# Optimization experiments

Measured on AMD Instinct MI355X. Metric: run time of the kernel, lower is better.

## Reference

```python
import jax, jax.numpy as jnp
import numpy as np

D_MODEL = 1024
NUM_HEADS = 16
HEAD_DIM = D_MODEL // NUM_HEADS


def setup_inputs() -> dict:
    key = jax.random.key(0)
    ks = jax.random.split(key, 11)
    B, S, D = 2, 2048, D_MODEL
    s = 1.0 / np.sqrt(D)
    return {
        "query": jax.random.normal(ks[0], (B, S, D), jnp.float32),
        "key": jax.random.normal(ks[1], (B, S, D), jnp.float32),
        "value": jax.random.normal(ks[2], (B, S, D), jnp.float32),
        "W_q": jax.random.normal(ks[3], (D, D), jnp.float32) * s,
        "b_q": jnp.zeros((D,), jnp.float32),
        "W_k": jax.random.normal(ks[4], (D, D), jnp.float32) * s,
        "b_k": jnp.zeros((D,), jnp.float32),
        "W_v": jax.random.normal(ks[5], (D, D), jnp.float32) * s,
        "b_v": jnp.zeros((D,), jnp.float32),
        "W_o": jax.random.normal(ks[6], (D, D), jnp.float32) * s,
        "b_o": jnp.zeros((D,), jnp.float32),
    }


def reference(query, key, value, W_q, b_q, W_k, b_k, W_v, b_v, W_o, b_o):
    B, S, D = query.shape
    H, Dh = NUM_HEADS, HEAD_DIM
    # linear projections then split heads: [B, S, D] -> [B, H, S, Dh]
    def split_heads(x):
        return x.reshape(B, -1, H, Dh).transpose(0, 2, 1, 3)
    Q = split_heads(query @ W_q.T + b_q)
    K = split_heads(key @ W_k.T + b_k)
    V = split_heads(value @ W_v.T + b_v)
    # NOTE: original scales by d_model**-0.5, not head_dim**-0.5
    scale = jnp.asarray(D, Q.dtype) ** -0.5
    scores = jnp.einsum("bhqd,bhkd->bhqk", Q, K) * scale
    attn = jax.nn.softmax(scores, axis=-1)  # includes max-subtraction stabilization
    out = jnp.einsum("bhqk,bhkd->bhqd", attn, V)
    out = out.transpose(0, 2, 1, 3).reshape(B, -1, D)
    return out @ W_o.T + b_o
```

## Files before the change

kernel.cpp:

```cpp
#include <hip/hip_runtime.h>
#include <stdint.h>


typedef unsigned short u16;
typedef short s16x8 __attribute__((ext_vector_type(8)));
typedef short s16x4 __attribute__((ext_vector_type(4)));
typedef float f32x4 __attribute__((ext_vector_type(4)));
typedef u16 u16x4 __attribute__((ext_vector_type(4)));

#define S_LEN 2048
#define DMODEL 1024
#define LOG2E 1.44269504088896340736f

__device__ __forceinline__ u16 f2bf(float f) {
  union { float f; uint32_t u; } v; v.f = f;
  return (u16)((v.u + 0x8000u) >> 16);
}

__device__ __forceinline__ s16x8 ld8f(const float* s) {
  f32x4 a = *(const f32x4*)s;
  f32x4 b = *(const f32x4*)(s + 4);
  s16x8 r;
  r[0] = (short)f2bf(a[0]); r[1] = (short)f2bf(a[1]);
  r[2] = (short)f2bf(a[2]); r[3] = (short)f2bf(a[3]);
  r[4] = (short)f2bf(b[0]); r[5] = (short)f2bf(b[1]);
  r[6] = (short)f2bf(b[2]); r[7] = (short)f2bf(b[3]);
  return r;
}

__device__ __forceinline__ void gl2lds16(const u16* g, u16* l) {
  __builtin_amdgcn_global_load_lds(
      (const __attribute__((address_space(1))) uint32_t*)g,
      (__attribute__((address_space(3))) uint32_t*)l, 16, 0, 0);
}

struct Cvt7 { const float* s[7]; u16* d[7]; int n[7]; };

__global__ __launch_bounds__(256) void cvt7(Cvt7 p) {
  const int z = blockIdx.y;
  const int idx = blockIdx.x * 256 + threadIdx.x;
  if (idx * 8 < p.n[z])
    *(s16x8*)(p.d[z] + (size_t)idx * 8) = ld8f(p.s[z] + (size_t)idx * 8);
}

struct GemmBatch {
  const u16* A[3]; const u16* W[3]; const float* Bv[3]; void* C[3];
};

template <bool OUT_F32>
__global__ __launch_bounds__(256) void gemm_bt(GemmBatch p, int M, int N, int K) {
  __shared__ u16 As[128 * 64];
  __shared__ u16 Ws[128 * 64];
  const int z = blockIdx.z;
  const u16* __restrict__ A      = p.A[z];
  const u16* __restrict__ W      = p.W[z];
  const float* __restrict__ bias = p.Bv[z];

  const int tid = threadIdx.x;
  const int wave = tid >> 6, lane = tid & 63;
  const int quad = lane >> 4, l16 = lane & 15;
  const int bm = blockIdx.y * 128, bn = blockIdx.x * 128;
  const int wr = (wave >> 1) * 64, wc = (wave & 1) * 64;
  const int sr8 = lane >> 3;
  const int slc = (lane & 7) ^ sr8;
  const int srow = wave * 8 + sr8;

  f32x4 acc[4][4];
#pragma unroll
  for (int i = 0; i < 4; i++)
#pragma unroll
    for (int j = 0; j < 4; j++) acc[i][j] = {0.f, 0.f, 0.f, 0.f};

  const u16* Ab = A + (size_t)bm * K;
  const u16* Wb = W + (size_t)bn * K;

  for (int kt = 0; kt < K; kt += 64) {
    __syncthreads();
#pragma unroll
    for (int i = 0; i < 4; i++)
      gl2lds16(Ab + (size_t)(i * 32 + srow) * K + kt + slc * 8,
               &As[(i * 32 + wave * 8) * 64]);
#pragma unroll
    for (int i = 0; i < 4; i++)
      gl2lds16(Wb + (size_t)(i * 32 + srow) * K + kt + slc * 8,
               &Ws[(i * 32 + wave * 8) * 64]);
    __syncthreads();

#pragma unroll
    for (int ks = 0; ks < 2; ks++) {
      const int ch = ks * 4 + quad;
      s16x8 a[4], b[4];
#pragma unroll
      for (int t = 0; t < 4; t++)
        a[t] = *(const s16x8*)&As[(wr + t * 16 + l16) * 64 + ((ch ^ (l16 & 7)) << 3)];
#pragma unroll
      for (int t = 0; t < 4; t++)
        b[t] = *(const s16x8*)&Ws[(wc + t * 16 + l16) * 64 + ((ch ^ (l16 & 7)) << 3)];
#pragma unroll
      for (int i = 0; i < 4; i++)
#pragma unroll
        for (int j = 0; j < 4; j++)
          acc[i][j] = __builtin_amdgcn_mfma_f32_16x16x32_bf16(a[i], b[j], acc[i][j], 0, 0, 0);
    }
  }

#pragma unroll
  for (int j = 0; j < 4; j++) {
    const int col = bn + wc + j * 16 + l16;
    const float bv = bias[col];
#pragma unroll
    for (int i = 0; i < 4; i++) {
      const int row0 = bm + wr + i * 16 + quad * 4;
#pragma unroll
      for (int r = 0; r < 4; r++) {
        const float val = acc[i][j][r] + bv;
        if (OUT_F32)
          ((float*)p.C[z])[(size_t)(row0 + r) * N + col] = val;
        else
          ((u16*)p.C[z])[(size_t)(row0 + r) * N + col] = f2bf(val);
      }
    }
  }
}

__global__ __launch_bounds__(256) void transpose_v(const u16* __restrict__ Vp,
                                                   u16* __restrict__ Vt) {
  __shared__ u16 t[64 * 72];
  const int tid = threadIdx.x;
  const int bh = blockIdx.y, b = bh >> 4, h = bh & 15;
  const int s0 = blockIdx.x * 64;
  const int r = tid >> 4, c4 = (tid & 15) * 4;
#pragma unroll
  for (int i = 0; i < 4; i++) {
    const int s = i * 16 + r;
    u16x4 v = *(const u16x4*)&Vp[(size_t)(b * S_LEN + s0 + s) * DMODEL + h * 64 + c4];
    *(u16x4*)&t[s * 72 + c4] = v;
  }
  __syncthreads();
#pragma unroll
  for (int i = 0; i < 4; i++) {
    const int d = i * 16 + r;
    u16x4 v;
    v.x = t[(c4 + 0) * 72 + d];
    v.y = t[(c4 + 1) * 72 + d];
    v.z = t[(c4 + 2) * 72 + d];
    v.w = t[(c4 + 3) * 72 + d];
    *(u16x4*)&Vt[(size_t)(bh * 64 + d) * S_LEN + s0 + c4] = v;
  }
}

__global__ __launch_bounds__(512, 2) void attn_kernel(const u16* __restrict__ Qp,
                                                      const u16* __restrict__ Kp,
                                                      const u16* __restrict__ Vt,
                                                      u16* __restrict__ AO) {
  __shared__ u16 Qs[128 * 64];
  __shared__ u16 Ks[128 * 64];
  __shared__ u16 Vs[64 * 128];

  const int tid = threadIdx.x;
  const int wave = tid >> 6, lane = tid & 63;
  const int quad = lane >> 4, l16 = lane & 15;
  const int bh = blockIdx.y, b = bh >> 4, h = bh & 15;
  const int s0 = blockIdx.x * 128;
  const float c = 0.03125f * LOG2E;

  const int sr = tid >> 3, sc8 = tid & 7;
  const int sxor = (sc8 ^ (sr & 7)) << 3;
  const int vr = tid >> 4, vc = tid & 15;
  const int vxor = (vc ^ (vr & 15)) << 3;

#pragma unroll
  for (int i = 0; i < 2; i++) {
    const int rr = i * 64 + sr;
    s16x8 qv = *(const s16x8*)(Qp + (size_t)(b * S_LEN + s0 + rr) * DMODEL + h * 64 + sc8 * 8);
    *(s16x8*)&Qs[rr * 64 + sxor] = qv;
  }
  __syncthreads();

  s16x8 aq[2];
#pragma unroll
  for (int ks = 0; ks < 2; ks++) {
    const int ch = ks * 4 + quad;
    aq[ks] = *(const s16x8*)&Qs[(wave * 16 + l16) * 64 + ((ch ^ (l16 & 7)) << 3)];
  }

  s16x8 kv[2], vv[2];
#pragma unroll
  for (int i = 0; i < 2; i++)
    kv[i] = *(const s16x8*)(Kp + (size_t)(b * S_LEN + i * 64 + sr) * DMODEL + h * 64 + sc8 * 8);
#pragma unroll
  for (int i = 0; i < 2; i++)
    vv[i] = *(const s16x8*)(Vt + (size_t)(bh * 64 + i * 32 + vr) * S_LEN + vc * 8);

  f32x4 o[4];
  float l_r = 0.f;
#pragma unroll
  for (int dt = 0; dt < 4; dt++) o[dt] = {0.f, 0.f, 0.f, 0.f};

  const f32x4 zf = {0.f, 0.f, 0.f, 0.f};

  for (int kt = 0; kt < S_LEN; kt += 128) {
    __syncthreads();
#pragma unroll
    for (int i = 0; i < 2; i++)
      *(s16x8*)&Ks[(i * 64 + sr) * 64 + sxor] = kv[i];
#pragma unroll
    for (int i = 0; i < 2; i++)
      *(s16x8*)&Vs[(i * 32 + vr) * 128 + vxor] = vv[i];
    __syncthreads();

    if (kt + 128 < S_LEN) {
      const int k2 = kt + 128;
#pragma unroll
      for (int i = 0; i < 2; i++)
        kv[i] = *(const s16x8*)(Kp + (size_t)(b * S_LEN + k2 + i * 64 + sr) * DMODEL + h * 64 + sc8 * 8);
#pragma unroll
      for (int i = 0; i < 2; i++)
        vv[i] = *(const s16x8*)(Vt + (size_t)(bh * 64 + i * 32 + vr) * S_LEN + k2 + vc * 8);
    }

#pragma unroll
    for (int kvt = 0; kvt < 8; kvt++) {
      const int krow = kvt * 16 + l16;
      s16x8 ak0 = *(const s16x8*)&Ks[krow * 64 + (((0 + quad) ^ (l16 & 7)) << 3)];
      s16x8 ak1 = *(const s16x8*)&Ks[krow * 64 + (((4 + quad) ^ (l16 & 7)) << 3)];
      f32x4 sA;
      sA = __builtin_amdgcn_mfma_f32_16x16x32_bf16(ak0, aq[0], zf, 0, 0, 0);
      sA = __builtin_amdgcn_mfma_f32_16x16x32_bf16(ak1, aq[1], sA, 0, 0, 0);

      s16x4 pf;
      float rs = 0.f;
#pragma unroll
      for (int r = 0; r < 4; r++) {
        const float p0 = exp2f(sA[r] * c);
        rs += p0;
        pf[r] = (short)f2bf(p0);
      }
      l_r += rs;

      const int ch = kvt * 2 + (quad >> 1);
#pragma unroll
      for (int dt = 0; dt < 4; dt++) {
        const int row = dt * 16 + l16;
        s16x4 bv = *(const s16x4*)&Vs[row * 128 + ((ch ^ l16) << 3) + (quad & 1) * 4];
        o[dt] = __builtin_amdgcn_mfma_f32_16x16x16bf16_1k(pf, bv, o[dt], 0, 0, 0);
      }
    }
  }

  l_r += __shfl_xor(l_r, 16);
  l_r += __shfl_xor(l_r, 32);
#pragma unroll
  for (int r = 0; r < 4; r++) {
    const float linv = 1.f / __shfl(l_r, quad * 4 + r);
    const int row = s0 + wave * 16 + quad * 4 + r;
#pragma unroll
    for (int dt = 0; dt < 4; dt++)
      AO[(size_t)(b * S_LEN + row) * DMODEL + h * 64 + dt * 16 + l16] =
          f2bf(o[dt][r] * linv);
  }
}

extern "C" void kernel_launch(void* const* d_in, const int* in_sizes, int n_in,
                              void* d_out, int out_size, void* d_ws, size_t ws_size,
                              hipStream_t stream) {
  const float* query = (const float*)d_in[0];
  const float* key_  = (const float*)d_in[1];
  const float* value = (const float*)d_in[2];
  const float* W_q = (const float*)d_in[3];
  const float* b_q = (const float*)d_in[4];
  const float* W_k = (const float*)d_in[5];
  const float* b_k = (const float*)d_in[6];
  const float* W_v = (const float*)d_in[7];
  const float* b_v = (const float*)d_in[8];
  const float* W_o = (const float*)d_in[9];
  const float* b_o = (const float*)d_in[10];
  float* out = (float*)d_out;

  const int M = 2 * S_LEN;
  const int N = DMODEL, K = DMODEL;
  const size_t WSZ = (size_t)DMODEL * DMODEL;
  const size_t SZ  = (size_t)M * DMODEL;

  u16* Wqb = (u16*)d_ws;
  u16* Wkb = Wqb + WSZ;
  u16* Wvb = Wkb + WSZ;
  u16* Wob = Wvb + WSZ;
  u16* Qa  = Wob + WSZ;
  u16* Ka  = Qa + SZ;
  u16* Va  = Ka + SZ;
  u16* Qp  = Va + SZ;
  u16* Kp  = Qp + SZ;
  u16* Vp  = Kp + SZ;
  u16* Vt  = Qa;
  u16* AO  = Qp;

  Cvt7 cw;
  cw.s[0] = W_q;   cw.d[0] = Wqb; cw.n[0] = (int)WSZ;
  cw.s[1] = W_k;   cw.d[1] = Wkb; cw.n[1] = (int)WSZ;
  cw.s[2] = W_v;   cw.d[2] = Wvb; cw.n[2] = (int)WSZ;
  cw.s[3] = W_o;   cw.d[3] = Wob; cw.n[3] = (int)WSZ;
  cw.s[4] = query; cw.d[4] = Qa;  cw.n[4] = (int)SZ;
  cw.s[5] = key_;  cw.d[5] = Ka;  cw.n[5] = (int)SZ;
  cw.s[6] = value; cw.d[6] = Va;  cw.n[6] = (int)SZ;
  cvt7<<<dim3((int)(SZ / 2048), 7), 256, 0, stream>>>(cw);

  GemmBatch p1;
  p1.A[0] = Qa; p1.W[0] = Wqb; p1.Bv[0] = b_q; p1.C[0] = Qp;
  p1.A[1] = Ka; p1.W[1] = Wkb; p1.Bv[1] = b_k; p1.C[1] = Kp;
  p1.A[2] = Va; p1.W[2] = Wvb; p1.Bv[2] = b_v; p1.C[2] = Vp;
  gemm_bt<false><<<dim3(N / 128, M / 128, 3), 256, 0, stream>>>(p1, M, N, K);

  transpose_v<<<dim3(S_LEN / 64, 32), 256, 0, stream>>>(Vp, Vt);

  attn_kernel<<<dim3(S_LEN / 128, 32), 512, 0, stream>>>(Qp, Kp, Vt, AO);

  GemmBatch p2;
  p2.A[0] = AO; p2.W[0] = Wob; p2.Bv[0] = b_o; p2.C[0] = out;
  p2.A[1] = AO; p2.W[1] = Wob; p2.Bv[1] = b_o; p2.C[1] = out;
  p2.A[2] = AO; p2.W[2] = Wob; p2.Bv[2] = b_o; p2.C[2] = out;
  gemm_bt<true><<<dim3(N / 128, M / 128, 1), 256, 0, stream>>>(p2, M, N, K);
}
```

Baseline: 255.1 us.

## Fuse V transpose into QKV GEMM epilogue and retile output projection

The QKV projection GEMM now writes the V projection already transposed, staging the tile through LDS in the epilogue and storing contiguous rows of Vt. This removes the separate transpose_v kernel and its round trip of V through global memory. The GEMM is templated on tile size, and the output projection switches to 64x64 tiles, giving four times as many blocks for better CU occupancy. The cost is extra LDS traffic and a sync in the V epilogue, and smaller tiles get less data reuse.

```diff
diff --git a/kernel.cpp b/kernel.cpp
--- a/kernel.cpp
+++ b/kernel.cpp
@@ -45,12 +45,21 @@
 
 struct GemmBatch {
   const u16* A[3]; const u16* W[3]; const float* Bv[3]; void* C[3];
+  u16* vt;
 };
 
-template <bool OUT_F32>
+template <int BM, int BN, bool OUT_F32, bool VT>
 __global__ __launch_bounds__(256) void gemm_bt(GemmBatch p, int M, int N, int K) {
-  __shared__ u16 As[128 * 64];
-  __shared__ u16 Ws[128 * 64];
+  static_assert(!VT || (BM == 128 && BN == 128), "VT epilogue assumes 128x128");
+  constexpr int MI = BM / 32, NJ = BN / 32;
+  constexpr int TS = BM + 8;
+  constexpr int AB = BM * 64 + BN * 64;
+  constexpr int TB = VT ? BN * TS : 0;
+  constexpr int SM = AB > TB ? AB : TB;
+  __shared__ u16 smem[SM];
+  u16* const As = smem;
+  u16* const Ws = smem + BM * 64;
+
   const int z = blockIdx.z;
   const u16* __restrict__ A      = p.A[z];
   const u16* __restrict__ W      = p.W[z];
@@ -59,17 +68,17 @@
   const int tid = threadIdx.x;
   const int wave = tid >> 6, lane = tid & 63;
   const int quad = lane >> 4, l16 = lane & 15;
-  const int bm = blockIdx.y * 128, bn = blockIdx.x * 128;
-  const int wr = (wave >> 1) * 64, wc = (wave & 1) * 64;
+  const int bm = blockIdx.y * BM, bn = blockIdx.x * BN;
+  const int wr = (wave >> 1) * (BM / 2), wc = (wave & 1) * (BN / 2);
   const int sr8 = lane >> 3;
   const int slc = (lane & 7) ^ sr8;
   const int srow = wave * 8 + sr8;
 
-  f32x4 acc[4][4];
-#pragma unroll
-  for (int i = 0; i < 4; i++)
-#pragma unroll
-    for (int j = 0; j < 4; j++) acc[i][j] = {0.f, 0.f, 0.f, 0.f};
+  f32x4 acc[MI][NJ];
+#pragma unroll
+  for (int i = 0; i < MI; i++)
+#pragma unroll
+    for (int j = 0; j < NJ; j++) acc[i][j] = {0.f, 0.f, 0.f, 0.f};
 
   const u16* Ab = A + (size_t)bm * K;
   const u16* Wb = W + (size_t)bn * K;
@@ -77,11 +86,11 @@
   for (int kt = 0; kt < K; kt += 64) {
     __syncthreads();
 #pragma unroll
-    for (int i = 0; i < 4; i++)
+    for (int i = 0; i < MI; i++)
       gl2lds16(Ab + (size_t)(i * 32 + srow) * K + kt + slc * 8,
                &As[(i * 32 + wave * 8) * 64]);
 #pragma unroll
-    for (int i = 0; i < 4; i++)
+    for (int i = 0; i < NJ; i++)
       gl2lds16(Wb + (size_t)(i * 32 + srow) * K + kt + slc * 8,
                &Ws[(i * 32 + wave * 8) * 64]);
     __syncthreads();
@@ -89,63 +98,64 @@
 #pragma unroll
     for (int ks = 0; ks < 2; ks++) {
       const int ch = ks * 4 + quad;
-      s16x8 a[4], b[4];
-#pragma unroll
-      for (int t = 0; t < 4; t++)
+      s16x8 a[MI], b[NJ];
+#pragma unroll
+      for (int t = 0; t < MI; t++)
         a[t] = *(const s16x8*)&As[(wr + t * 16 + l16) * 64 + ((ch ^ (l16 & 7)) << 3)];
 #pragma unroll
-      for (int t = 0; t < 4; t++)
+      for (int t = 0; t < NJ; t++)
         b[t] = *(const s16x8*)&Ws[(wc + t * 16 + l16) * 64 + ((ch ^ (l16 & 7)) << 3)];
 #pragma unroll
-      for (int i = 0; i < 4; i++)
-#pragma unroll
-        for (int j = 0; j < 4; j++)
+      for (int i = 0; i < MI; i++)
+#pragma unroll
+        for (int j = 0; j < NJ; j++)
           acc[i][j] = __builtin_amdgcn_mfma_f32_16x16x32_bf16(a[i], b[j], acc[i][j], 0, 0, 0);
     }
   }
 
-#pragma unroll
-  for (int j = 0; j < 4; j++) {
-    const int col = bn + wc + j * 16 + l16;
-    const float bv = bias[col];
-#pragma unroll
-    for (int i = 0; i < 4; i++) {
-      const int row0 = bm + wr + i * 16 + quad * 4;
-#pragma unroll
-      for (int r = 0; r < 4; r++) {
-        const float val = acc[i][j][r] + bv;
-        if (OUT_F32)
-          ((float*)p.C[z])[(size_t)(row0 + r) * N + col] = val;
-        else
-          ((u16*)p.C[z])[(size_t)(row0 + r) * N + col] = f2bf(val);
+  if (VT && z == 2) {
+    __syncthreads();
+    u16* const T = smem;
+#pragma unroll
+    for (int j = 0; j < NJ; j++) {
+      const int c = wc + j * 16 + l16;
+      const float bv = bias[bn + c];
+#pragma unroll
+      for (int i = 0; i < MI; i++) {
+        const int r0 = wr + i * 16 + quad * 4;
+        u16x4 t4;
+#pragma unroll
+        for (int r = 0; r < 4; r++) t4[r] = f2bf(acc[i][j][r] + bv);
+        *(u16x4*)&T[c * TS + r0] = t4;
       }
     }
-  }
-}
-
-__global__ __launch_bounds__(256) void transpose_v(const u16* __restrict__ Vp,
-                                                   u16* __restrict__ Vt) {
-  __shared__ u16 t[64 * 72];
-  const int tid = threadIdx.x;
-  const int bh = blockIdx.y, b = bh >> 4, h = bh & 15;
-  const int s0 = blockIdx.x * 64;
-  const int r = tid >> 4, c4 = (tid & 15) * 4;
-#pragma unroll
-  for (int i = 0; i < 4; i++) {
-    const int s = i * 16 + r;
-    u16x4 v = *(const u16x4*)&Vp[(size_t)(b * S_LEN + s0 + s) * DMODEL + h * 64 + c4];
-    *(u16x4*)&t[s * 72 + c4] = v;
-  }
-  __syncthreads();
-#pragma unroll
-  for (int i = 0; i < 4; i++) {
-    const int d = i * 16 + r;
-    u16x4 v;
-    v.x = t[(c4 + 0) * 72 + d];
-    v.y = t[(c4 + 1) * 72 + d];
-    v.z = t[(c4 + 2) * 72 + d];
-    v.w = t[(c4 + 3) * 72 + d];
-    *(u16x4*)&Vt[(size_t)(bh * 64 + d) * S_LEN + s0 + c4] = v;
+    __syncthreads();
+    const int c = tid >> 1, half = tid & 1;
+    const int b_ = bm >> 11;
+    const int sb = (bm & 2047) + half * 64;
+    u16* dst = p.vt + (size_t)(b_ * 1024 + bn + c) * S_LEN + sb;
+    const u16* srcT = &T[c * TS + half * 64];
+#pragma unroll
+    for (int k = 0; k < 8; k++)
+      *(s16x8*)(dst + k * 8) = *(const s16x8*)(srcT + k * 8);
+  } else {
+#pragma unroll
+    for (int j = 0; j < NJ; j++) {
+      const int col = bn + wc + j * 16 + l16;
+      const float bv = bias[col];
+#pragma unroll
+      for (int i = 0; i < MI; i++) {
+        const int row0 = bm + wr + i * 16 + quad * 4;
+#pragma unroll
+        for (int r = 0; r < 4; r++) {
+          const float val = acc[i][j][r] + bv;
+          if (OUT_F32)
+            ((float*)p.C[z])[(size_t)(row0 + r) * N + col] = val;
+          else
+            ((u16*)p.C[z])[(size_t)(row0 + r) * N + col] = f2bf(val);
+        }
+      }
+    }
   }
 }
 
@@ -291,8 +301,7 @@
   u16* Va  = Ka + SZ;
   u16* Qp  = Va + SZ;
   u16* Kp  = Qp + SZ;
-  u16* Vp  = Kp + SZ;
-  u16* Vt  = Qa;
+  u16* Vt  = Kp + SZ;
   u16* AO  = Qp;
 
   Cvt7 cw;
@@ -308,10 +317,9 @@
   GemmBatch p1;
   p1.A[0] = Qa; p1.W[0] = Wqb; p1.Bv[0] = b_q; p1.C[0] = Qp;
   p1.A[1] = Ka; p1.W[1] = Wkb; p1.Bv[1] = b_k; p1.C[1] = Kp;
-  p1.A[2] = Va; p1.W[2] = Wvb; p1.Bv[2] = b_v; p1.C[2] = Vp;
-  gemm_bt<false><<<dim3(N / 128, M / 128, 3), 256, 0, stream>>>(p1, M, N, K);
-
-  transpose_v<<<dim3(S_LEN / 64, 32), 256, 0, stream>>>(Vp, Vt);
+  p1.A[2] = Va; p1.W[2] = Wvb; p1.Bv[2] = b_v; p1.C[2] = Vt;
+  p1.vt = Vt;
+  gemm_bt<128, 128, false, true><<<dim3(N / 128, M / 128, 3), 256, 0, stream>>>(p1, M, N, K);
 
   attn_kernel<<<dim3(S_LEN / 128, 32), 512, 0, stream>>>(Qp, Kp, Vt, AO);
 
@@ -319,5 +327,6 @@
   p2.A[0] = AO; p2.W[0] = Wob; p2.Bv[0] = b_o; p2.C[0] = out;
   p2.A[1] = AO; p2.W[1] = Wob; p2.Bv[1] = b_o; p2.C[1] = out;
   p2.A[2] = AO; p2.W[2] = Wob; p2.Bv[2] = b_o; p2.C[2] = out;
-  gemm_bt<true><<<dim3(N / 128, M / 128, 1), 256, 0, stream>>>(p2, M, N, K);
-}
+  p2.vt = nullptr;
+  gemm_bt<64, 64, true, false><<<dim3(N / 64, M / 64, 1), 256, 0, stream>>>(p2, M, N, K);
+}
```

Measured after the change: 241.2 us. 1.06x faster.
